# Performance work log

Hardware: AMD Instinct MI355X
Metric: run time of the kernel (lower is better)

The kernel has to match this reference:

```python
import jax, jax.numpy as jnp
import numpy as np

B, L, NW, H, HID, E, NL, DL = 32, 1024, 512, 768, 384, 4, 12, 128


def setup_inputs() -> dict:
    key = jax.random.key(0)
    ks = jax.random.split(key, 16)
    f = lambda k, s: jax.random.normal(k, s, dtype=jnp.float32) * 0.02
    z = lambda s: jnp.zeros(s, jnp.float32)
    return {
        "token_embs": jax.random.normal(ks[0], (B, L, H), dtype=jnp.float32),
        "word_maps": jnp.sort(jax.random.randint(ks[1], (B, L), 0, NW), axis=-1),
        "lang_ids": jax.random.randint(ks[2], (B,), 0, NL),
        # BiLSTM params (PyTorch gate order i,f,g,o packed along dim 0)
        "Wih_f": f(ks[3], (4 * HID, H)), "Whh_f": f(ks[4], (4 * HID, HID)),
        "bih_f": z((4 * HID,)), "bhh_f": z((4 * HID,)),
        "Wih_b": f(ks[5], (4 * HID, H)), "Whh_b": f(ks[6], (4 * HID, HID)),
        "bih_b": z((4 * HID,)), "bhh_b": z((4 * HID,)),
        "proj_W": f(ks[7], (H, 2 * HID)), "proj_b": z((H,)),
        "lang_table": f(ks[8], (NL, DL)),
        "gate_W1": f(ks[9], (H, H + DL)), "gate_b1": z((H,)),
        "gate_W2": f(ks[10], (E, H)), "gate_b2": z((E,)),
        # stacked expert heads: row i is expert i's (H,1) linear
        "ef_W": f(ks[11], (E, H)), "ef_b": z((E,)),
        "ed_W": f(ks[12], (E, H)), "ed_b": z((E,)),
    }


def _seg_mean(embs, wmap):
    # embs: [L, H], wmap: [L] -> [NW, H] per-word mean of subword embeddings
    sums = jax.ops.segment_sum(embs, wmap, num_segments=NW)
    cnt = jax.ops.segment_sum(jnp.ones(embs.shape[:1], embs.dtype), wmap, num_segments=NW)
    return sums / jnp.maximum(cnt, 1.0)[:, None]


def _lstm(x, Wih, Whh, bih, bhh, reverse):
    # x: [B, T, H] -> hidden states [B, T, HID]; gate order i,f,g,o
    def step(carry, xg):
        h, c = carry
        g = xg + h @ Whh.T + bhh
        i, fg, gg, o = jnp.split(g, 4, axis=-1)
        c = jax.nn.sigmoid(fg) * c + jax.nn.sigmoid(i) * jnp.tanh(gg)
        h = jax.nn.sigmoid(o) * jnp.tanh(c)
        return (h, c), h
    xg = jnp.swapaxes(x @ Wih.T + bih, 0, 1)  # [T, B, 4*HID], input proj hoisted
    init = (jnp.zeros((x.shape[0], Whh.shape[1]), x.dtype),) * 2
    _, hs = jax.lax.scan(step, init, xg, reverse=reverse)
    return jnp.swapaxes(hs, 0, 1)


def reference(token_embs, word_maps, lang_ids, Wih_f, Whh_f, bih_f, bhh_f,
              Wih_b, Whh_b, bih_b, bhh_b, proj_W, proj_b, lang_table,
              gate_W1, gate_b1, gate_W2, gate_b2, ef_W, ef_b, ed_W, ed_b):
    # subword -> word segment-mean pooling, batched
    word_embs = jax.vmap(_seg_mean)(token_embs, word_maps)          # [B, NW, H]
    hf = _lstm(word_embs, Wih_f, Whh_f, bih_f, bhh_f, False)        # [B, NW, HID]
    hb = _lstm(word_embs, Wih_b, Whh_b, bih_b, bhh_b, True)         # [B, NW, HID]
    seq = jnp.concatenate([hf, hb], axis=-1) @ proj_W.T + proj_b    # [B, NW, H]
    # dropout omitted (eval mode)
    gate_in = jnp.concatenate([token_embs[:, 0], lang_table[lang_ids]], axis=-1)  # [B, H+DL]
    gate = jax.nn.softmax(
        jax.nn.relu(gate_in @ gate_W1.T + gate_b1) @ gate_W2.T + gate_b2, axis=-1)  # [B, E]
    fix = jnp.einsum('bwe,be->bw', seq @ ef_W.T + ef_b, gate)       # [B, NW]
    dur = jnp.einsum('bwe,be->bw', seq @ ed_W.T + ed_b, gate)       # [B, NW]
    return (fix, dur)
```

## Files before the change

kernel.cpp:

```cpp
#include <hip/hip_runtime.h>
#include <stdint.h>

#define BB 32
#define LL 1024
#define NW 512
#define HH 768
#define HID 384
#define G4 1536
#define EE 4
#define DLL 128
#define GIN 896
#define CWG 12
#define WGC 32
#define HPAD 392

typedef __attribute__((ext_vector_type(8))) short short8;
typedef __attribute__((ext_vector_type(4))) float f32x4;
typedef __attribute__((ext_vector_type(2))) float f32x2;

__device__ __forceinline__ float bf2f(short s){
  union { unsigned int u; float f; } v; v.u = ((unsigned int)(unsigned short)s) << 16; return v.f;
}
__device__ __forceinline__ short f2bf(float f){
  union { float f; unsigned int u; } v; v.f = f;
  unsigned int r = v.u + 0x7fffu + ((v.u >> 16) & 1u);
  return (short)(r >> 16);
}
__device__ __forceinline__ float sigm(float x){ return 1.f / (1.f + __expf(-x)); }

__global__ void k_zero(int* flags){
  int i = blockIdx.x * 256 + threadIdx.x;
  if (i < 2 * NW) flags[i] = 0;
}

__global__ void k_f2bf(const float* in, short* out, int n){
  int i = blockIdx.x * blockDim.x + threadIdx.x;
  int st = gridDim.x * blockDim.x;
  for (; i < n; i += st) out[i] = f2bf(in[i]);
}

__global__ __launch_bounds__(256) void k_segmean(const float* __restrict__ tok,
                                                 const int* __restrict__ wmap,
                                                 short* __restrict__ we_bf){
  int blk = blockIdx.x;
  int b = blk >> 9;
  int w = blk & 511;
  const int* m = wmap + b * LL;
  int lo = 0, hi = LL;
  while (lo < hi){ int mid = (lo + hi) >> 1; if (m[mid] < w) lo = mid + 1; else hi = mid; }
  int s = lo;
  int lo2 = s, hi2 = LL;
  while (lo2 < hi2){ int mid = (lo2 + hi2) >> 1; if (m[mid] <= w) lo2 = mid + 1; else hi2 = mid; }
  int e = lo2;
  float cnt = (float)(e - s);
  float denom = fmaxf(cnt, 1.f);
  for (int j = threadIdx.x; j < HH; j += 256){
    float acc = 0.f;
    for (int r = s; r < e; ++r) acc += tok[((size_t)b * LL + r) * HH + j];
    we_bf[((size_t)b * NW + w) * HH + j] = f2bf(acc / denom);
  }
}

__global__ __launch_bounds__(256) void k_gemm_bt(const short* __restrict__ Abf,
                                                 const short* __restrict__ Wbf,
                                                 const float* __restrict__ b1,
                                                 const float* __restrict__ b2,
                                                 float* __restrict__ Cf,
                                                 int M, int N, int K){
  __shared__ __attribute__((aligned(16))) short As[128 * 32];
  __shared__ __attribute__((aligned(16))) short Bs[128 * 32];
  int ntiles = N >> 7;
  int m0 = (blockIdx.x / ntiles) << 7;
  int n0 = (blockIdx.x % ntiles) << 7;
  int tid = threadIdx.x, lane = tid & 63, wv = tid >> 6;
  int wm = (wv >> 1) << 6, wn = (wv & 1) << 6;
  f32x4 acc[4][4] = {};
  for (int kk = 0; kk < K; kk += 32){
#pragma unroll
    for (int q = 0; q < 2; ++q){
      int e = (q * 256 + tid) * 8;
      int row = e >> 5, col = e & 31;
      *(short8*)(As + e) = *(const short8*)(Abf + (size_t)(m0 + row) * K + kk + col);
      *(short8*)(Bs + e) = *(const short8*)(Wbf + (size_t)(n0 + row) * K + kk + col);
    }
    __syncthreads();
    short8 af[4], bfr[4];
#pragma unroll
    for (int x = 0; x < 4; ++x){
      af[x]  = *(const short8*)(As + (wm + x * 16 + (lane & 15)) * 32 + ((lane >> 4) << 3));
      bfr[x] = *(const short8*)(Bs + (wn + x * 16 + (lane & 15)) * 32 + ((lane >> 4) << 3));
    }
#pragma unroll
    for (int x = 0; x < 4; ++x)
#pragma unroll
      for (int y = 0; y < 4; ++y)
        acc[x][y] = __builtin_amdgcn_mfma_f32_16x16x32_bf16(af[x], bfr[y], acc[x][y], 0, 0, 0);
    __syncthreads();
  }
#pragma unroll
  for (int x = 0; x < 4; ++x)
#pragma unroll
    for (int y = 0; y < 4; ++y)
#pragma unroll
      for (int i = 0; i < 4; ++i){
        int mm = m0 + wm + x * 16 + ((lane >> 4) << 2) + i;
        int nn = n0 + wn + y * 16 + (lane & 15);
        Cf[(size_t)mm * N + nn] = acc[x][y][i] + b1[nn] + b2[nn];
      }
}

__global__ __launch_bounds__(512) void k_lstm(const float* __restrict__ xg_f,
                                              const float* __restrict__ xg_b,
                                              const short* __restrict__ whh_f,
                                              const short* __restrict__ whh_b,
                                              short* __restrict__ hbuf,
                                              short* __restrict__ hcat,
                                              int* __restrict__ flags){
  int bx = blockIdx.x;
  int dir = bx / CWG;
  int cg  = bx % CWG;
  int tid = threadIdx.x, lane = tid & 63, wv = tid >> 6;
  const float* xg  = dir ? xg_b : xg_f;
  const short* whh = dir ? whh_b : whh_f;
  int g  = wv >> 1;
  int nh = wv & 1;
  int jbase = g * HID + cg * WGC + nh * 16;

  short8 bfrag[12];
  {
    const short* wr = whh + (size_t)(jbase + (lane & 15)) * HID + ((lane >> 4) << 3);
#pragma unroll
    for (int ks = 0; ks < 12; ++ks) bfrag[ks] = *(const short8*)(wr + ks * 32);
  }

  __shared__ __attribute__((aligned(16))) short hs[32 * HPAD];
  __shared__ float pre[4][BB][WGC];

  float c0 = 0.f, c1 = 0.f;
  int eb = tid >> 4, ecp = (tid & 15) * 2;
  int crow = tid >> 4, cidx = tid & 15;
  int* flg = flags + dir * NW;
  short* hb0 = hbuf + (size_t)dir * 2 * BB * HID;

  for (int t = 0; t < NW; ++t){
    int t_act = dir ? (NW - 1 - t) : t;
    float xgv[8];
#pragma unroll
    for (int mt = 0; mt < 2; ++mt)
#pragma unroll
      for (int i = 0; i < 4; ++i){
        int bb = mt * 16 + ((lane >> 4) << 2) + i;
        xgv[mt * 4 + i] = xg[((size_t)bb * NW + t_act) * G4 + jbase + (lane & 15)];
      }
    f32x4 acc0 = {}, acc1 = {};
    if (t > 0){
      if (tid == 0){
        while (__hip_atomic_load(&flg[t - 1], __ATOMIC_RELAXED, __HIP_MEMORY_SCOPE_AGENT) < CWG)
          __builtin_amdgcn_s_sleep(1);
      }
      __syncthreads();
      const short* hp = hb0 + ((t - 1) & 1) * BB * HID;
      const unsigned long long* src = (const unsigned long long*)(hp + (size_t)crow * HID);
#pragma unroll
      for (int q = 0; q < 6; ++q){
        unsigned long long v = __hip_atomic_load(src + cidx * 6 + q,
                                                 __ATOMIC_RELAXED, __HIP_MEMORY_SCOPE_AGENT);
        *(unsigned long long*)(hs + crow * HPAD + cidx * 24 + q * 4) = v;
      }
      __syncthreads();
#pragma unroll
      for (int ks = 0; ks < 12; ++ks){
        short8 a0 = *(const short8*)(hs + (lane & 15) * HPAD        + ks * 32 + ((lane >> 4) << 3));
        short8 a1 = *(const short8*)(hs + ((lane & 15) + 16) * HPAD + ks * 32 + ((lane >> 4) << 3));
        acc0 = __builtin_amdgcn_mfma_f32_16x16x32_bf16(a0, bfrag[ks], acc0, 0, 0, 0);
        acc1 = __builtin_amdgcn_mfma_f32_16x16x32_bf16(a1, bfrag[ks], acc1, 0, 0, 0);
      }
    }
#pragma unroll
    for (int i = 0; i < 4; ++i){
      int b0 = ((lane >> 4) << 2) + i;
      pre[g][b0][nh * 16 + (lane & 15)]      = acc0[i] + xgv[i];
      pre[g][b0 + 16][nh * 16 + (lane & 15)] = acc1[i] + xgv[4 + i];
    }
    __syncthreads();
    f32x2 gi = *(f32x2*)&pre[0][eb][ecp];
    f32x2 gf = *(f32x2*)&pre[1][eb][ecp];
    f32x2 gg = *(f32x2*)&pre[2][eb][ecp];
    f32x2 go = *(f32x2*)&pre[3][eb][ecp];
    c0 = sigm(gf.x) * c0 + sigm(gi.x) * tanhf(gg.x);
    float h0 = sigm(go.x) * tanhf(c0);
    c1 = sigm(gf.y) * c1 + sigm(gi.y) * tanhf(gg.y);
    float h1 = sigm(go.y) * tanhf(c1);
    unsigned int packed = (unsigned int)(unsigned short)f2bf(h0) |
                          ((unsigned int)(unsigned short)f2bf(h1) << 16);
    short* hw = hb0 + (t & 1) * BB * HID;
    __hip_atomic_store((unsigned int*)(hw + eb * HID + cg * WGC + ecp), packed,
                       __ATOMIC_RELAXED, __HIP_MEMORY_SCOPE_AGENT);
    *(unsigned int*)(hcat + ((size_t)eb * NW + t_act) * HH + dir * HID + cg * WGC + ecp) = packed;
    asm volatile("s_waitcnt vmcnt(0)" ::: "memory");
    __syncthreads();
    if (tid == 0)
      __hip_atomic_fetch_add(&flg[t], 1, __ATOMIC_RELAXED, __HIP_MEMORY_SCOPE_AGENT);
  }
}

__global__ __launch_bounds__(256) void k_gate(const float* __restrict__ tok,
                                              const int* __restrict__ lids,
                                              const float* __restrict__ ltab,
                                              const float* __restrict__ W1,
                                              const float* __restrict__ b1v,
                                              const float* __restrict__ W2,
                                              const float* __restrict__ b2v,
                                              float* __restrict__ gate){
  __shared__ float gin[GIN];
  __shared__ float hid[HH];
  __shared__ float pr[EE];
  int b = blockIdx.x, tid = threadIdx.x;
  int lid = lids[b];
  for (int i = tid; i < GIN; i += 256)
    gin[i] = (i < HH) ? tok[(size_t)b * LL * HH + i] : ltab[lid * DLL + (i - HH)];
  __syncthreads();
  for (int j = tid; j < HH; j += 256){
    float a = b1v[j];
    const float* wr = W1 + (size_t)j * GIN;
    for (int k = 0; k < GIN; ++k) a += gin[k] * wr[k];
    hid[j] = fmaxf(a, 0.f);
  }
  __syncthreads();
  int wv = tid >> 6, lane = tid & 63;
  if (wv < EE){
    float p = 0.f;
    for (int k = lane; k < HH; k += 64) p += hid[k] * W2[wv * HH + k];
#pragma unroll
    for (int off = 32; off; off >>= 1) p += __shfl_down(p, off);
    if (lane == 0) pr[wv] = p + b2v[wv];
  }
  __syncthreads();
  if (tid == 0){
    float mx = fmaxf(fmaxf(pr[0], pr[1]), fmaxf(pr[2], pr[3]));
    float s = 0.f, ex[EE];
    for (int e2 = 0; e2 < EE; ++e2){ ex[e2] = __expf(pr[e2] - mx); s += ex[e2]; }
    for (int e2 = 0; e2 < EE; ++e2) gate[b * EE + e2] = ex[e2] / s;
  }
}

__global__ __launch_bounds__(256) void k_headpre(const float* __restrict__ efW,
                                                 const float* __restrict__ efb,
                                                 const float* __restrict__ edW,
                                                 const float* __restrict__ edb,
                                                 const float* __restrict__ projW,
                                                 const float* __restrict__ projb,
                                                 float* __restrict__ Acomb,
                                                 float* __restrict__ Ccomb){
  int head = blockIdx.x >> 2, e2 = blockIdx.x & 3, tid = threadIdx.x;
  const float* Wv = head ? edW : efW;
  const float* bv = head ? edb : efb;
  __shared__ float wrow[HH];
  for (int i = tid; i < HH; i += 256) wrow[i] = Wv[e2 * HH + i];
  __syncthreads();
  for (int c = tid; c < HH; c += 256){
    float a = 0.f;
    for (int h2 = 0; h2 < HH; ++h2) a += wrow[h2] * projW[(size_t)h2 * HH + c];
    Acomb[(head * 4 + e2) * HH + c] = a;
  }
  int wv = tid >> 6, lane = tid & 63;
  if (wv == 0){
    float p = 0.f;
    for (int k = lane; k < HH; k += 64) p += wrow[k] * projb[k];
#pragma unroll
    for (int off = 32; off; off >>= 1) p += __shfl_down(p, off);
    if (lane == 0) Ccomb[head * 4 + e2] = p + bv[e2];
  }
}

__global__ __launch_bounds__(256) void k_heads(const short* __restrict__ hcat,
                                               const float* __restrict__ Acomb,
                                               const float* __restrict__ Ccomb,
                                               const float* __restrict__ gate,
                                               float* __restrict__ outp){
  __shared__ float Al[8 * HH];
  int tid = threadIdx.x;
  for (int i = tid; i < 8 * HH; i += 256) Al[i] = Acomb[i];
  __syncthreads();
  int wv = tid >> 6, lane = tid & 63;
  int bw = blockIdx.x * 4 + wv;
  const short* hr = hcat + (size_t)bw * HH;
  float hv[12];
#pragma unroll
  for (int j = 0; j < 12; ++j) hv[j] = bf2f(hr[lane + 64 * j]);
  float dsum[8];
#pragma unroll
  for (int v = 0; v < 8; ++v){
    float p = 0.f;
#pragma unroll
    for (int j = 0; j < 12; ++j) p += hv[j] * Al[v * HH + lane + 64 * j];
#pragma unroll
    for (int off = 32; off; off >>= 1) p += __shfl_xor(p, off);
    dsum[v] = p;
  }
  if (lane == 0){
    int b = bw >> 9;
    float fx = 0.f, du = 0.f;
#pragma unroll
    for (int e2 = 0; e2 < 4; ++e2){
      float g = gate[b * 4 + e2];
      fx += g * (dsum[e2]     + Ccomb[e2]);
      du += g * (dsum[4 + e2] + Ccomb[4 + e2]);
    }
    outp[bw] = fx;
    outp[BB * NW + bw] = du;
  }
}

extern "C" void kernel_launch(void* const* d_in, const int* in_sizes, int n_in,
                              void* d_out, int out_size, void* d_ws, size_t ws_size,
                              hipStream_t stream){
  const float* tok   = (const float*)d_in[0];
  const int*   wmap  = (const int*)d_in[1];
  const int*   lids  = (const int*)d_in[2];
  const float* Wih_f = (const float*)d_in[3];
  const float* Whh_f = (const float*)d_in[4];
  const float* bih_f = (const float*)d_in[5];
  const float* bhh_f = (const float*)d_in[6];
  const float* Wih_b = (const float*)d_in[7];
  const float* Whh_b = (const float*)d_in[8];
  const float* bih_b = (const float*)d_in[9];
  const float* bhh_b = (const float*)d_in[10];
  const float* projW = (const float*)d_in[11];
  const float* projb = (const float*)d_in[12];
  const float* ltab  = (const float*)d_in[13];
  const float* gW1   = (const float*)d_in[14];
  const float* gb1   = (const float*)d_in[15];
  const float* gW2   = (const float*)d_in[16];
  const float* gb2   = (const float*)d_in[17];
  const float* efW   = (const float*)d_in[18];
  const float* efb   = (const float*)d_in[19];
  const float* edW   = (const float*)d_in[20];
  const float* edb   = (const float*)d_in[21];
  float* outp = (float*)d_out;

  char* ws = (char*)d_ws;
  size_t off = 0;
  auto alloc = [&](size_t bytes) -> char* {
    char* p = ws + off;
    off = (off + bytes + 255) & ~(size_t)255;
    return p;
  };
  short* we_bf   = (short*)alloc((size_t)BB * NW * HH * 2);
  short* wihf_bf = (short*)alloc((size_t)G4 * HH * 2);
  short* wihb_bf = (short*)alloc((size_t)G4 * HH * 2);
  short* whhf_bf = (short*)alloc((size_t)G4 * HID * 2);
  short* whhb_bf = (short*)alloc((size_t)G4 * HID * 2);
  float* xg_f    = (float*)alloc((size_t)BB * NW * G4 * 4);
  float* xg_b    = (float*)alloc((size_t)BB * NW * G4 * 4);
  short* hcat    = (short*)alloc((size_t)BB * NW * HH * 2);
  short* hbuf    = (short*)alloc((size_t)2 * 2 * BB * HID * 2);
  int*   flags   = (int*)alloc((size_t)2 * NW * 4);
  float* gateb   = (float*)alloc((size_t)BB * EE * 4);
  float* Acomb   = (float*)alloc((size_t)8 * HH * 4);
  float* Ccomb   = (float*)alloc((size_t)8 * 4);

  k_zero<<<4, 256, 0, stream>>>(flags);
  k_f2bf<<<1024, 256, 0, stream>>>(Wih_f, wihf_bf, G4 * HH);
  k_f2bf<<<1024, 256, 0, stream>>>(Wih_b, wihb_bf, G4 * HH);
  k_f2bf<<<512, 256, 0, stream>>>(Whh_f, whhf_bf, G4 * HID);
  k_f2bf<<<512, 256, 0, stream>>>(Whh_b, whhb_bf, G4 * HID);
  k_segmean<<<BB * NW, 256, 0, stream>>>(tok, wmap, we_bf);
  k_gemm_bt<<<(BB * NW / 128) * (G4 / 128), 256, 0, stream>>>(we_bf, wihf_bf, bih_f, bhh_f, xg_f, BB * NW, G4, HH);
  k_gemm_bt<<<(BB * NW / 128) * (G4 / 128), 256, 0, stream>>>(we_bf, wihb_bf, bih_b, bhh_b, xg_b, BB * NW, G4, HH);
  k_gate<<<BB, 256, 0, stream>>>(tok, lids, ltab, gW1, gb1, gW2, gb2, gateb);
  k_headpre<<<8, 256, 0, stream>>>(efW, efb, edW, edb, projW, projb, Acomb, Ccomb);
  k_lstm<<<2 * CWG, 512, 0, stream>>>(xg_f, xg_b, whhf_bf, whhb_bf, hbuf, hcat, flags);
  k_heads<<<(BB * NW) / 4, 256, 0, stream>>>(hcat, Acomb, Ccomb, gateb, outp);
}
```

Baseline: 2.322 ms.

## Use per-workgroup flags, wave-level polling, and bulk h loads in LSTM recurrence

The recurrent LSTM kernel drops the single atomic counter per timestep. Each workgroup now stores its own flag, and every wave polls all 12 flags in parallel with __all, so thread 0 no longer spins before a barrier. The previous hidden state is read with three coherent dwordx4 loads per thread instead of six 64-bit atomic loads. Workgroup 0 writes the full gathered h row into hcat for the previous step, replacing the per-workgroup scattered hcat stores. The input-projection GEMM also switches to global_load_lds direct-to-LDS copies, the pre-activation LDS array is padded to 36 columns, and the flag buffer is enlarged, at the cost of more flag memory and busier polling traffic.

```diff
diff --git a/kernel.cpp b/kernel.cpp
--- a/kernel.cpp
+++ b/kernel.cpp
@@ -28,9 +28,15 @@
 }
 __device__ __forceinline__ float sigm(float x){ return 1.f / (1.f + __expf(-x)); }
 
-__global__ void k_zero(int* flags){
+__device__ __forceinline__ void gload16(const void* g, void* l){
+  __builtin_amdgcn_global_load_lds(
+      (const __attribute__((address_space(1))) unsigned int*)g,
+      (__attribute__((address_space(3))) unsigned int*)l, 16, 0, 0);
+}
+
+__global__ void k_zero(int* flags, int n){
   int i = blockIdx.x * 256 + threadIdx.x;
-  if (i < 2 * NW) flags[i] = 0;
+  if (i < n) flags[i] = 0;
 }
 
 __global__ void k_f2bf(const float* in, short* out, int n){
@@ -78,10 +84,10 @@
   for (int kk = 0; kk < K; kk += 32){
 #pragma unroll
     for (int q = 0; q < 2; ++q){
-      int e = (q * 256 + tid) * 8;
-      int row = e >> 5, col = e & 31;
-      *(short8*)(As + e) = *(const short8*)(Abf + (size_t)(m0 + row) * K + kk + col);
-      *(short8*)(Bs + e) = *(const short8*)(Wbf + (size_t)(n0 + row) * K + kk + col);
+      int e = q * 256 + tid;
+      int row = e >> 2, col = (e & 3) << 3;
+      gload16(Abf + (size_t)(m0 + row) * K + kk + col, As + e * 8);
+      gload16(Wbf + (size_t)(n0 + row) * K + kk + col, Bs + e * 8);
     }
     __syncthreads();
     short8 af[4], bfr[4];
@@ -134,12 +140,12 @@
   }
 
   __shared__ __attribute__((aligned(16))) short hs[32 * HPAD];
-  __shared__ float pre[4][BB][WGC];
+  __shared__ float pre[4][BB][36];
 
   float c0 = 0.f, c1 = 0.f;
   int eb = tid >> 4, ecp = (tid & 15) * 2;
-  int crow = tid >> 4, cidx = tid & 15;
-  int* flg = flags + dir * NW;
+  int pc = lane & 15;
+  int* flgD = flags + dir * NW * 16;
   short* hb0 = hbuf + (size_t)dir * 2 * BB * HID;
 
   for (int t = 0; t < NW; ++t){
@@ -154,18 +160,37 @@
       }
     f32x4 acc0 = {}, acc1 = {};
     if (t > 0){
-      if (tid == 0){
-        while (__hip_atomic_load(&flg[t - 1], __ATOMIC_RELAXED, __HIP_MEMORY_SCOPE_AGENT) < CWG)
-          __builtin_amdgcn_s_sleep(1);
-      }
-      __syncthreads();
+      const int* fl = flgD + (t - 1) * 16;
+      for (;;){
+        int v = __hip_atomic_load(&fl[pc], __ATOMIC_RELAXED, __HIP_MEMORY_SCOPE_AGENT);
+        if (__all(v != 0 || pc >= CWG)) break;
+      }
       const short* hp = hb0 + ((t - 1) & 1) * BB * HID;
-      const unsigned long long* src = (const unsigned long long*)(hp + (size_t)crow * HID);
-#pragma unroll
-      for (int q = 0; q < 6; ++q){
-        unsigned long long v = __hip_atomic_load(src + cidx * 6 + q,
-                                                 __ATOMIC_RELAXED, __HIP_MEMORY_SCOPE_AGENT);
-        *(unsigned long long*)(hs + crow * HPAD + cidx * 24 + q * 4) = v;
+      short8 sv0, sv1, sv2;
+      {
+        const short* s0 = hp + (0 * 512 + tid) * 8;
+        const short* s1 = hp + (1 * 512 + tid) * 8;
+        const short* s2 = hp + (2 * 512 + tid) * 8;
+        asm volatile("global_load_dwordx4 %0, %1, off sc0 sc1" : "=v"(sv0) : "v"(s0) : "memory");
+        asm volatile("global_load_dwordx4 %0, %1, off sc0 sc1" : "=v"(sv1) : "v"(s1) : "memory");
+        asm volatile("global_load_dwordx4 %0, %1, off sc0 sc1" : "=v"(sv2) : "v"(s2) : "memory");
+        asm volatile("s_waitcnt vmcnt(0)" ::: "memory");
+      }
+      short8 svv[3] = {sv0, sv1, sv2};
+#pragma unroll
+      for (int q = 0; q < 3; ++q){
+        int gi = q * 512 + tid;
+        int b = gi / 48, rem = gi % 48;
+        *(short8*)(hs + b * HPAD + rem * 8) = svv[q];
+      }
+      if (cg == 0){
+        int tprev = dir ? (NW - t) : (t - 1);
+#pragma unroll
+        for (int q = 0; q < 3; ++q){
+          int gi = q * 512 + tid;
+          int b = gi / 48, rem = gi % 48;
+          *(short8*)(hcat + ((size_t)b * NW + tprev) * HH + dir * HID + rem * 8) = svv[q];
+        }
       }
       __syncthreads();
 #pragma unroll
@@ -183,24 +208,25 @@
       pre[g][b0 + 16][nh * 16 + (lane & 15)] = acc1[i] + xgv[4 + i];
     }
     __syncthreads();
-    f32x2 gi = *(f32x2*)&pre[0][eb][ecp];
-    f32x2 gf = *(f32x2*)&pre[1][eb][ecp];
-    f32x2 gg = *(f32x2*)&pre[2][eb][ecp];
-    f32x2 go = *(f32x2*)&pre[3][eb][ecp];
-    c0 = sigm(gf.x) * c0 + sigm(gi.x) * tanhf(gg.x);
-    float h0 = sigm(go.x) * tanhf(c0);
-    c1 = sigm(gf.y) * c1 + sigm(gi.y) * tanhf(gg.y);
-    float h1 = sigm(go.y) * tanhf(c1);
+    f32x2 gi2 = *(f32x2*)&pre[0][eb][ecp];
+    f32x2 gf2 = *(f32x2*)&pre[1][eb][ecp];
+    f32x2 gg2 = *(f32x2*)&pre[2][eb][ecp];
+    f32x2 go2 = *(f32x2*)&pre[3][eb][ecp];
+    c0 = sigm(gf2.x) * c0 + sigm(gi2.x) * tanhf(gg2.x);
+    float h0 = sigm(go2.x) * tanhf(c0);
+    c1 = sigm(gf2.y) * c1 + sigm(gi2.y) * tanhf(gg2.y);
+    float h1 = sigm(go2.y) * tanhf(c1);
     unsigned int packed = (unsigned int)(unsigned short)f2bf(h0) |
                           ((unsigned int)(unsigned short)f2bf(h1) << 16);
     short* hw = hb0 + (t & 1) * BB * HID;
     __hip_atomic_store((unsigned int*)(hw + eb * HID + cg * WGC + ecp), packed,
                        __ATOMIC_RELAXED, __HIP_MEMORY_SCOPE_AGENT);
-    *(unsigned int*)(hcat + ((size_t)eb * NW + t_act) * HH + dir * HID + cg * WGC + ecp) = packed;
+    if (t == NW - 1)
+      *(unsigned int*)(hcat + ((size_t)eb * NW + t_act) * HH + dir * HID + cg * WGC + ecp) = packed;
     asm volatile("s_waitcnt vmcnt(0)" ::: "memory");
     __syncthreads();
     if (tid == 0)
-      __hip_atomic_fetch_add(&flg[t], 1, __ATOMIC_RELAXED, __HIP_MEMORY_SCOPE_AGENT);
+      __hip_atomic_store(&flgD[t * 16 + cg], 1, __ATOMIC_RELAXED, __HIP_MEMORY_SCOPE_AGENT);
   }
 }
 
@@ -355,12 +381,12 @@
   float* xg_b    = (float*)alloc((size_t)BB * NW * G4 * 4);
   short* hcat    = (short*)alloc((size_t)BB * NW * HH * 2);
   short* hbuf    = (short*)alloc((size_t)2 * 2 * BB * HID * 2);
-  int*   flags   = (int*)alloc((size_t)2 * NW * 4);
+  int*   flags   = (int*)alloc((size_t)2 * NW * 16 * 4);
   float* gateb   = (float*)alloc((size_t)BB * EE * 4);
   float* Acomb   = (float*)alloc((size_t)8 * HH * 4);
   float* Ccomb   = (float*)alloc((size_t)8 * 4);
 
-  k_zero<<<4, 256, 0, stream>>>(flags);
+  k_zero<<<(2 * NW * 16 + 255) / 256, 256, 0, stream>>>(flags, 2 * NW * 16);
   k_f2bf<<<1024, 256, 0, stream>>>(Wih_f, wihf_bf, G4 * HH);
   k_f2bf<<<1024, 256, 0, stream>>>(Wih_b, wihb_bf, G4 * HH);
   k_f2bf<<<512, 256, 0, stream>>>(Whh_f, whhf_bf, G4 * HID);
```

New measurement: 2.176 ms. -6.3%, faster.
